# Kernel tuning notes

Hardware: AMD Instinct MI355X
Metric: run time of the kernel (lower is better)

The kernel has to match this reference:

```python
import jax, jax.numpy as jnp
import numpy as np

NUM_ROUTING = 3


def squash(s):
    # NOTE: original torch code sums the squared norm over axis=2 (the
    # out-capsule axis of s_j [B,1,O,Do]), NOT the feature axis. Faithful copy.
    norm = jnp.sum(s * s, axis=2, keepdims=True)
    scale = norm / (1.0 + norm) / jnp.sqrt(norm + 1e-9)
    return scale * s


def setup_inputs() -> dict:
    key = jax.random.key(0)
    k1, k2 = jax.random.split(key)
    B, N, Di, O, Do = 64, 8192, 8, 10, 16
    x = jax.random.normal(k1, (B, N, Di), dtype=jnp.float32)
    W = 0.01 * jax.random.normal(k2, (1, N, O, Do, Di), dtype=jnp.float32)
    return {"x": x, "W": W}


def reference(x, W):
    # x: [B, N, Di]; W: [1, N, O, Do, Di]
    N = x.shape[1]
    O = W.shape[2]
    # u_hat = W @ x per (n, o): [B, N, O, Do]
    u_hat = jnp.einsum('nodi,bni->bnod', W[0], x)
    b_ij = jnp.zeros((1, N, O, 1), dtype=x.dtype)
    v_j = None
    for r in range(NUM_ROUTING):
        c_ij = jax.nn.softmax(b_ij, axis=2)            # softmax over out caps
        s_j = jnp.sum(c_ij * u_hat, axis=1, keepdims=True)  # [B,1,O,Do]
        v_j = squash(s_j)
        if r < NUM_ROUTING - 1:
            # agreement: broadcasts b_ij to [B,N,O,1] after first update
            b_ij = b_ij + jnp.sum(u_hat * v_j, axis=-1, keepdims=True)
    return v_j[:, 0]  # [B, O, Do]
```

## Files before the change

### kernel.cpp

```cpp
#include <hip/hip_runtime.h>

typedef unsigned int u32;
typedef unsigned short u16;
typedef _Float16 h2 __attribute__((ext_vector_type(2)));
typedef _Float16 h4 __attribute__((ext_vector_type(4)));
typedef float f4 __attribute__((ext_vector_type(4)));

#define B_ 64
#define N_ 8192
#define DI 8
#define O_ 10
#define DO_ 16
#define OD 160
#define NB 256
#define NCH 32
#define WROW (OD * DI)
#define WLN (NCH * WROW)
#define XROW 264
#define CSTR 164

#define NCHUNK 8
#define CHN 2
#define NCHK (NCHUNK / CHN)
#define CHH (CHN * WROW)

static __device__ __forceinline__ h2 pkrtz(float a, float b) {
    return __builtin_bit_cast(h2, __builtin_amdgcn_cvt_pkrtz(a, b));
}

static __device__ __forceinline__ h2 hsum4(h2 v, int a32) {
    int pi = __builtin_bit_cast(int, v);
    h2 pk = v + __builtin_bit_cast(h2, __builtin_amdgcn_ds_swizzle(pi, 0x401F));
    pi = __builtin_bit_cast(int, pk);
    pk = pk + __builtin_bit_cast(h2, __builtin_amdgcn_ds_bpermute(a32, pi));
    return pk;
}

static __device__ __forceinline__ void gbar_arrive(u32* cnt, u32* flag, u32 k) {
    __syncthreads();
    if (threadIdx.x == 0) {
        const u32 old = __hip_atomic_fetch_add(cnt, 1u, __ATOMIC_RELEASE,
                                               __HIP_MEMORY_SCOPE_AGENT);
        if (old == k * NB - 1)
            __hip_atomic_store(flag, k, __ATOMIC_RELEASE, __HIP_MEMORY_SCOPE_AGENT);
    }
}
static __device__ __forceinline__ void gbar_wait(u32* flag, u32 k) {
    if (threadIdx.x == 0) {
        while (__hip_atomic_load(flag, __ATOMIC_RELAXED, __HIP_MEMORY_SCOPE_AGENT) < k)
            __builtin_amdgcn_s_sleep(8);
        (void)__hip_atomic_load(flag, __ATOMIC_ACQUIRE, __HIP_MEMORY_SCOPE_AGENT);
    }
    __syncthreads();
}

__global__ __launch_bounds__(512, 2)
void caps_fused(const float* __restrict__ Xf, const float* __restrict__ Wf,
                u32* bar, float* __restrict__ V0f, u16* __restrict__ Vb,
                _Float16* __restrict__ P, float* __restrict__ out) {
    __shared__ _Float16 wl[WLN];
    __shared__ _Float16 xl[B_ * XROW];
    __shared__ float cmb[B_ * CSTR];

    const int tid  = threadIdx.x;
    const int lane = tid & 63;
    const int c    = lane & 15;
    const int hh   = lane >> 4;
    const int w    = __builtin_amdgcn_readfirstlane(tid >> 6);
    const int tau  = w & 3, eta = w >> 2;
    const int b    = tau * 16 + c;
    const int bid  = blockIdx.x;
    const int nb   = bid * NCH;
    const int a32  = (lane ^ 32) << 2;
    const int ioff = (hh < 2) ? 4 * hh : 0;

    u32* cnt  = bar;
    u32* flag = bar + 32;

    {
        const float* src = Wf + (size_t)nb * WROW;
        float4 wv[20];
        #pragma unroll
        for (int k = 0; k < 20; ++k) wv[k] = *(const float4*)(src + (tid + k * 512) * 4);
        const float* xs = Xf + ((size_t)(tid >> 3) * N_ + nb) * DI;
        float4 xv[8];
        #pragma unroll
        for (int k = 0; k < 8; ++k) xv[k] = *(const float4*)(xs + ((tid & 7) + k * 8) * 4);
        #pragma unroll
        for (int k = 0; k < 20; ++k) {
            h2 lo = pkrtz(wv[k].x, wv[k].y), hi = pkrtz(wv[k].z, wv[k].w);
            h4 hv; hv[0] = lo[0]; hv[1] = lo[1]; hv[2] = hi[0]; hv[3] = hi[1];
            *(h4*)&wl[(tid + k * 512) * 4] = hv;
        }
        #pragma unroll
        for (int k = 0; k < 8; ++k) {
            const int pos = ((tid & 7) + k * 8) * 4;
            h2 lo = pkrtz(xv[k].x, xv[k].y), hi = pkrtz(xv[k].z, xv[k].w);
            h4 hv; hv[0] = lo[0]; hv[1] = lo[1]; hv[2] = hi[0]; hv[3] = hi[1];
            *(h4*)&xl[(tid >> 3) * XROW + pos] = hv;
        }
    }
    __syncthreads();

    const f4 fz = {0.f, 0.f, 0.f, 0.f};
    f4 acc[O_], vv[O_];
    const _Float16* xrow = xl + b * XROW + ioff;

    auto loadvv = [&]() {
        const _Float16* vp = (const _Float16*)Vb + (size_t)b * OD + 4 * hh;
        #pragma unroll
        for (int oo = 0; oo < O_; ++oo) {
            const h4 hv = *(const h4*)(vp + oo * DO_);
            vv[oo][0] = (float)hv[0]; vv[oo][1] = (float)hv[1];
            vv[oo][2] = (float)hv[2]; vv[oo][3] = (float)hv[3];
        }
    };

    auto step1 = [&](int sn) {
        h4 bf = {(_Float16)0.f, (_Float16)0.f, (_Float16)0.f, (_Float16)0.f};
        if (hh < 2) bf = *(const h4*)(xrow + sn * 8);
        const _Float16* wr = wl + sn * WROW + c * DI + ioff;
        f4 u[O_];
        #pragma unroll
        for (int oo = 0; oo < O_; ++oo) {
            h4 af = {(_Float16)0.f, (_Float16)0.f, (_Float16)0.f, (_Float16)0.f};
            if (hh < 2) af = *(const h4*)(wr + oo * (DO_ * DI));
            u[oo] = __builtin_amdgcn_mfma_f32_16x16x16f16(af, bf, fz, 0, 0, 0);
        }
        float tex[O_];
        #pragma unroll
        for (int q = 0; q < 5; ++q) {
            const int o0 = 2 * q, o1 = 2 * q + 1;
            const float p0 = u[o0][0]*vv[o0][0] + u[o0][1]*vv[o0][1]
                           + u[o0][2]*vv[o0][2] + u[o0][3]*vv[o0][3];
            const float p1 = u[o1][0]*vv[o1][0] + u[o1][1]*vv[o1][1]
                           + u[o1][2]*vv[o1][2] + u[o1][3]*vv[o1][3];
            const h2 pk = hsum4(pkrtz(p0, p1), a32);
            tex[o0] = __expf((float)pk[0]);
            tex[o1] = __expf((float)pk[1]);
        }
        const float den = (((tex[0] + tex[1]) + (tex[2] + tex[3]))
                         + ((tex[4] + tex[5]) + (tex[6] + tex[7])))
                         + (tex[8] + tex[9]);
        const float rinv = 1.0f / den;
        #pragma unroll
        for (int oo = 0; oo < O_; ++oo) {
            const float co = tex[oo] * rinv;
            acc[oo][0] = fmaf(co, u[oo][0], acc[oo][0]);
            acc[oo][1] = fmaf(co, u[oo][1], acc[oo][1]);
            acc[oo][2] = fmaf(co, u[oo][2], acc[oo][2]);
            acc[oo][3] = fmaf(co, u[oo][3], acc[oo][3]);
        }
    };

    auto epi = [&](float sc) {
        if (eta == 1) {
            #pragma unroll
            for (int oo = 0; oo < O_; ++oo)
                *(f4*)&cmb[b * CSTR + oo * DO_ + 4 * hh] = acc[oo];
        }
        __syncthreads();
        if (eta == 0) {
            _Float16* my = P + (size_t)bid * (B_ * OD) + (size_t)b * OD;
            #pragma unroll
            for (int oo = 0; oo < O_; ++oo) {
                const f4 t = acc[oo] + *(const f4*)&cmb[b * CSTR + oo * DO_ + 4 * hh];
                h4 hq;
                hq[0] = (_Float16)(sc * t[0]); hq[1] = (_Float16)(sc * t[1]);
                hq[2] = (_Float16)(sc * t[2]); hq[3] = (_Float16)(sc * t[3]);
                *(h4*)(my + oo * DO_ + 4 * hh) = hq;
            }
        }
    };

    auto reduceF = [&](int r) {
        float* sg = cmb;
        float* ss = cmb + 512;
        float* sca = cmb + 704;
        if (tid < 480) {
            const int g = tid / 160, od = tid - g * 160;
            float a2 = 0.0f;
            const _Float16* p0 = P + (size_t)bid * OD + od;
            #pragma unroll 8
            for (int p = g; p < NB; p += 3)
                a2 += (float)p0[(size_t)p * (B_ * OD)];
            sg[g * 160 + od] = a2;
        }
        __syncthreads();
        if (tid < 160) ss[tid] = sg[tid] + sg[160 + tid] + sg[320 + tid];
        __syncthreads();
        if (tid < 16) {
            float nrm = 0.0f;
            #pragma unroll
            for (int o = 0; o < O_; ++o) { const float x = ss[o * DO_ + tid]; nrm = fmaf(x, x, nrm); }
            sca[tid] = nrm / (1.0f + nrm) * rsqrtf(nrm + 1e-9f);
        }
        __syncthreads();
        if (tid < 160) {
            const float v = ss[tid] * sca[tid & 15];
            const int idx = bid * OD + tid;
            if (r == 0) {
                V0f[idx] = v;
                _Float16 hcv = (_Float16)v;
                Vb[idx] = __builtin_bit_cast(u16, hcv);
            } else if (r == 1) {
                _Float16 hcv = (_Float16)(V0f[idx] + v);
                Vb[idx] = __builtin_bit_cast(u16, hcv);
            } else {
                out[idx] = v;
            }
        }
        __syncthreads();
    };

    #pragma unroll
    for (int oo = 0; oo < O_; ++oo) acc[oo] = fz;
    #pragma unroll 1
    for (int st = 0; st < 16; ++st) {
        const int sn = eta * 16 + st;
        h4 bf = {(_Float16)0.f, (_Float16)0.f, (_Float16)0.f, (_Float16)0.f};
        if (hh < 2) bf = *(const h4*)(xrow + sn * 8);
        const _Float16* wr = wl + sn * WROW + c * DI + ioff;
        #pragma unroll
        for (int oo = 0; oo < O_; ++oo) {
            h4 af = {(_Float16)0.f, (_Float16)0.f, (_Float16)0.f, (_Float16)0.f};
            if (hh < 2) af = *(const h4*)(wr + oo * (DO_ * DI));
            acc[oo] = __builtin_amdgcn_mfma_f32_16x16x16f16(af, bf, acc[oo], 0, 0, 0);
        }
    }
    epi(0.1f);
    gbar_arrive(cnt, flag, 1); gbar_wait(flag, 1);
    if (bid < B_) reduceF(0);
    gbar_arrive(cnt, flag, 2); gbar_wait(flag, 2);
    loadvv();

    #pragma unroll
    for (int oo = 0; oo < O_; ++oo) acc[oo] = fz;
    #pragma unroll 1
    for (int st = 0; st < 16; ++st) step1(eta * 16 + st);
    epi(1.0f);
    gbar_arrive(cnt, flag, 3); gbar_wait(flag, 3);
    if (bid < B_) reduceF(1);
    gbar_arrive(cnt, flag, 4); gbar_wait(flag, 4);
    loadvv();

    #pragma unroll
    for (int oo = 0; oo < O_; ++oo) acc[oo] = fz;
    #pragma unroll 1
    for (int st = 0; st < 16; ++st) step1(eta * 16 + st);
    epi(1.0f);

    gbar_arrive(cnt, flag, 5);
    if (bid < B_) {
        gbar_wait(flag, 5);
        reduceF(2);
    }
}

template <int PHASE, int TAIL>
__global__ __launch_bounds__(256, 3)
void caps_pass(const float* __restrict__ Xf, const float* __restrict__ Wf,
               const u16* __restrict__ Vb, float* __restrict__ Sout,
               _Float16* __restrict__ Sh) {
    __shared__ _Float16 stage[2 * CHH];

    const int tid  = threadIdx.x;
    const int lane = tid & 63;
    const int c    = lane & 15;
    const int hh   = lane >> 4;
    const int tau  = __builtin_amdgcn_readfirstlane(tid >> 6);
    const int b    = tau * 16 + c;
    const int nb   = blockIdx.x * NCHUNK;
    const int a32  = (lane ^ 32) << 2;

    int off[5];
    #pragma unroll
    for (int k = 0; k < 5; ++k) off[k] = (tid + k * 256) * 2;

    float2 st[5];
    {
        const float* src = Wf + (size_t)nb * WROW;
        #pragma unroll
        for (int k = 0; k < 5; ++k) st[k] = *(const float2*)(src + off[k]);
        #pragma unroll
        for (int k = 0; k < 5; ++k)
            *(h2*)&stage[off[k]] = pkrtz(st[k].x, st[k].y);
    }

    f4 vv[O_];
    if (PHASE > 0) {
        const _Float16* vp = (const _Float16*)Vb + (size_t)b * OD + 4 * hh;
        #pragma unroll
        for (int oo = 0; oo < O_; ++oo) {
            const h4 hv = *(const h4*)(vp + oo * DO_);
            vv[oo][0] = (float)hv[0]; vv[oo][1] = (float)hv[1];
            vv[oo][2] = (float)hv[2]; vv[oo][3] = (float)hv[3];
        }
    }

    const f4 fz = {0.f, 0.f, 0.f, 0.f};
    f4 acc[O_];
    #pragma unroll
    for (int oo = 0; oo < O_; ++oo) acc[oo] = fz;

    const int ioff = (hh < 2) ? 4 * hh : 0;
    const float* xb = Xf + ((size_t)b * N_ + nb) * DI + ioff;
    float4 xcur = *(const float4*)xb;

    __syncthreads();

    #pragma unroll 1
    for (int ch = 0; ch < NCHK; ++ch) {
        if (ch < NCHK - 1) {
            const float* src = Wf + (size_t)(nb + (ch + 1) * CHN) * WROW;
            #pragma unroll
            for (int k = 0; k < 5; ++k) st[k] = *(const float2*)(src + off[k]);
        }
        const _Float16* wb = stage + (ch & 1) * CHH;

        #pragma unroll
        for (int kk = 0; kk < CHN; ++kk) {
            const int s = ch * CHN + kk;
            float4 xnext = xcur;
            if (s < NCHUNK - 1)
                xnext = *(const float4*)(xb + (size_t)(s + 1) * DI);

            h4 bf = {(_Float16)0.f, (_Float16)0.f, (_Float16)0.f, (_Float16)0.f};
            if (hh < 2) {
                const h2 lo = pkrtz(xcur.x, xcur.y);
                const h2 hi = pkrtz(xcur.z, xcur.w);
                bf[0] = lo[0]; bf[1] = lo[1]; bf[2] = hi[0]; bf[3] = hi[1];
            }
            xcur = xnext;

            const _Float16* wr = wb + kk * WROW + c * DI + ioff;
            f4 u[O_];
            #pragma unroll
            for (int oo = 0; oo < O_; ++oo) {
                h4 af = {(_Float16)0.f, (_Float16)0.f, (_Float16)0.f, (_Float16)0.f};
                if (hh < 2) af = *(const h4*)(wr + oo * (DO_ * DI));
                if (PHASE == 0) {
                    acc[oo] = __builtin_amdgcn_mfma_f32_16x16x16f16(af, bf, acc[oo], 0, 0, 0);
                } else {
                    u[oo] = __builtin_amdgcn_mfma_f32_16x16x16f16(af, bf, fz, 0, 0, 0);
                }
            }

            if (PHASE > 0) {
                float tex[O_];
                #pragma unroll
                for (int q = 0; q < 5; ++q) {
                    const int o0 = 2 * q, o1 = 2 * q + 1;
                    const float p0 = u[o0][0]*vv[o0][0] + u[o0][1]*vv[o0][1]
                                   + u[o0][2]*vv[o0][2] + u[o0][3]*vv[o0][3];
                    const float p1 = u[o1][0]*vv[o1][0] + u[o1][1]*vv[o1][1]
                                   + u[o1][2]*vv[o1][2] + u[o1][3]*vv[o1][3];
                    const h2 pk = hsum4(pkrtz(p0, p1), a32);
                    tex[o0] = __expf((float)pk[0]);
                    tex[o1] = __expf((float)pk[1]);
                }
                const float den = (((tex[0] + tex[1]) + (tex[2] + tex[3]))
                                 + ((tex[4] + tex[5]) + (tex[6] + tex[7])))
                                 + (tex[8] + tex[9]);
                const float rinv = 1.0f / den;
                #pragma unroll
                for (int oo = 0; oo < O_; ++oo) {
                    const float co = tex[oo] * rinv;
                    acc[oo][0] = fmaf(co, u[oo][0], acc[oo][0]);
                    acc[oo][1] = fmaf(co, u[oo][1], acc[oo][1]);
                    acc[oo][2] = fmaf(co, u[oo][2], acc[oo][2]);
                    acc[oo][3] = fmaf(co, u[oo][3], acc[oo][3]);
                }
            }
        }

        if (ch < NCHK - 1) {
            _Float16* dst = stage + ((ch + 1) & 1) * CHH;
            #pragma unroll
            for (int k = 0; k < 5; ++k)
                *(h2*)&dst[off[k]] = pkrtz(st[k].x, st[k].y);
        }
        __syncthreads();
    }

    const float sc = (PHASE == 0) ? 0.1f : 1.0f;
    {
        float* Sg = Sout + (size_t)b * OD;
        #pragma unroll
        for (int oo = 0; oo < O_; ++oo) {
            atomicAdd(&Sg[oo * DO_ + 4 * hh + 0], sc * acc[oo][0]);
            atomicAdd(&Sg[oo * DO_ + 4 * hh + 1], sc * acc[oo][1]);
            atomicAdd(&Sg[oo * DO_ + 4 * hh + 2], sc * acc[oo][2]);
            atomicAdd(&Sg[oo * DO_ + 4 * hh + 3], sc * acc[oo][3]);
        }
    }
    (void)Sh;
}

template <int PHASE>
__global__ __launch_bounds__(1024)
void caps_finalize(float* __restrict__ S, float* __restrict__ V0f,
                   u16* __restrict__ Vb, float* __restrict__ out) {
    const int tid = threadIdx.x;
    const int b = tid >> 4, d = tid & 15;
    float sv[O_];
    float norm = 0.0f;
    #pragma unroll
    for (int o = 0; o < O_; ++o) {
        sv[o] = S[b * OD + o * DO_ + d];
        norm = fmaf(sv[o], sv[o], norm);
    }
    const float scale = norm / (1.0f + norm) * rsqrtf(norm + 1e-9f);
    #pragma unroll
    for (int o = 0; o < O_; ++o) {
        const int idx = b * OD + o * DO_ + d;
        const float v = scale * sv[o];
        if (PHASE == 0) {
            V0f[idx] = v;
            _Float16 hcv = (_Float16)v;
            Vb[idx] = __builtin_bit_cast(u16, hcv);
            S[idx] = 0.0f;
        } else if (PHASE == 1) {
            _Float16 hcv = (_Float16)(V0f[idx] + v);
            Vb[idx] = __builtin_bit_cast(u16, hcv);
            S[idx] = 0.0f;
        } else {
            out[idx] = v;
        }
    }
}

extern "C" void kernel_launch(void* const* d_in, const int* in_sizes, int n_in,
                              void* d_out, int out_size, void* d_ws, size_t ws_size,
                              hipStream_t stream) {
    const float* Xf = (const float*)d_in[0];
    const float* Wf = (const float*)d_in[1];
    float* out = (float*)d_out;

    const size_t velems = (size_t)B_ * OD;
    float* V0f = (float*)d_ws;
    u16* Vb = (u16*)(V0f + velems);
    u32* bar = (u32*)((char*)d_ws + 61440);
    const size_t pbase = 61696;
    const size_t need = pbase + (size_t)NB * velems * 2;

    if (ws_size >= need) {
        _Float16* P = (_Float16*)((char*)d_ws + pbase);
        (void)hipMemsetAsync(bar, 0, 256, stream);
        caps_fused<<<dim3(NB), dim3(512), 0, stream>>>(Xf, Wf, bar, V0f, Vb, P, out);
    } else {
        float* S = (float*)((char*)d_ws + pbase);
        const dim3 grid(N_ / NCHUNK), blk(256), one(1), fblk(1024);
        (void)hipMemsetAsync(S, 0, velems * sizeof(float), stream);
        caps_pass<0, 2><<<grid, blk, 0, stream>>>(Xf, Wf, nullptr, S, nullptr);
        caps_finalize<0><<<one, fblk, 0, stream>>>(S, V0f, Vb, nullptr);
        caps_pass<1, 2><<<grid, blk, 0, stream>>>(Xf, Wf, Vb, S, nullptr);
        caps_finalize<1><<<one, fblk, 0, stream>>>(S, V0f, Vb, nullptr);
        caps_pass<1, 2><<<grid, blk, 0, stream>>>(Xf, Wf, Vb, S, nullptr);
        caps_finalize<2><<<one, fblk, 0, stream>>>(S, nullptr, nullptr, out);
    }
}
```

Measured before the change: 203.9 us.

## Double grid to 512 blocks with half chunk per block and tree barrier

```diff
diff --git a/kernel.cpp b/kernel.cpp
--- a/kernel.cpp
+++ b/kernel.cpp
@@ -12,12 +12,12 @@
 #define O_ 10
 #define DO_ 16
 #define OD 160
-#define NB 256
-#define NCH 32
+#define NB2 512
+#define NCH 16
 #define WROW (OD * DI)
 #define WLN (NCH * WROW)
-#define XROW 264
-#define CSTR 164
+#define XROWH 136
+#define CSTRH 164
 
 #define NCHUNK 8
 #define CHN 2
@@ -36,17 +36,25 @@
     return pk;
 }
 
-static __device__ __forceinline__ void gbar_arrive(u32* cnt, u32* flag, u32 k) {
+static __device__ __forceinline__ void gbar_arrive(u32* bar, u32 k) {
     __syncthreads();
     if (threadIdx.x == 0) {
-        const u32 old = __hip_atomic_fetch_add(cnt, 1u, __ATOMIC_RELEASE,
-                                               __HIP_MEMORY_SCOPE_AGENT);
-        if (old == k * NB - 1)
-            __hip_atomic_store(flag, k, __ATOMIC_RELEASE, __HIP_MEMORY_SCOPE_AGENT);
-    }
-}
-static __device__ __forceinline__ void gbar_wait(u32* flag, u32 k) {
+        u32* leaf = bar + (blockIdx.x & 7) * 32;
+        u32* root = bar + 8 * 32;
+        u32* flag = bar + 9 * 32;
+        const u32 lo = __hip_atomic_fetch_add(leaf, 1u, __ATOMIC_RELEASE,
+                                              __HIP_MEMORY_SCOPE_AGENT);
+        if (lo == k * (NB2 / 8) - 1) {
+            const u32 ro = __hip_atomic_fetch_add(root, 1u, __ATOMIC_RELEASE,
+                                                  __HIP_MEMORY_SCOPE_AGENT);
+            if (ro == k * 8 - 1)
+                __hip_atomic_store(flag, k, __ATOMIC_RELEASE, __HIP_MEMORY_SCOPE_AGENT);
+        }
+    }
+}
+static __device__ __forceinline__ void gbar_wait(u32* bar, u32 k) {
     if (threadIdx.x == 0) {
+        u32* flag = bar + 9 * 32;
         while (__hip_atomic_load(flag, __ATOMIC_RELAXED, __HIP_MEMORY_SCOPE_AGENT) < k)
             __builtin_amdgcn_s_sleep(8);
         (void)__hip_atomic_load(flag, __ATOMIC_ACQUIRE, __HIP_MEMORY_SCOPE_AGENT);
@@ -54,13 +62,13 @@
     __syncthreads();
 }
 
-__global__ __launch_bounds__(512, 2)
+__global__ __launch_bounds__(512, 4)
 void caps_fused(const float* __restrict__ Xf, const float* __restrict__ Wf,
                 u32* bar, float* __restrict__ V0f, u16* __restrict__ Vb,
                 _Float16* __restrict__ P, float* __restrict__ out) {
     __shared__ _Float16 wl[WLN];
-    __shared__ _Float16 xl[B_ * XROW];
-    __shared__ float cmb[B_ * CSTR];
+    __shared__ _Float16 xl[B_ * XROWH];
+    __shared__ alignas(16) _Float16 cmbh[B_ * CSTRH];
 
     const int tid  = threadIdx.x;
     const int lane = tid & 63;
@@ -74,37 +82,34 @@
     const int a32  = (lane ^ 32) << 2;
     const int ioff = (hh < 2) ? 4 * hh : 0;
 
-    u32* cnt  = bar;
-    u32* flag = bar + 32;
-
     {
         const float* src = Wf + (size_t)nb * WROW;
-        float4 wv[20];
-        #pragma unroll
-        for (int k = 0; k < 20; ++k) wv[k] = *(const float4*)(src + (tid + k * 512) * 4);
+        float4 wv[10];
+        #pragma unroll
+        for (int k = 0; k < 10; ++k) wv[k] = *(const float4*)(src + (tid + k * 512) * 4);
         const float* xs = Xf + ((size_t)(tid >> 3) * N_ + nb) * DI;
-        float4 xv[8];
-        #pragma unroll
-        for (int k = 0; k < 8; ++k) xv[k] = *(const float4*)(xs + ((tid & 7) + k * 8) * 4);
-        #pragma unroll
-        for (int k = 0; k < 20; ++k) {
+        float4 xv[4];
+        #pragma unroll
+        for (int k = 0; k < 4; ++k) xv[k] = *(const float4*)(xs + ((tid & 7) + k * 8) * 4);
+        #pragma unroll
+        for (int k = 0; k < 10; ++k) {
             h2 lo = pkrtz(wv[k].x, wv[k].y), hi = pkrtz(wv[k].z, wv[k].w);
             h4 hv; hv[0] = lo[0]; hv[1] = lo[1]; hv[2] = hi[0]; hv[3] = hi[1];
             *(h4*)&wl[(tid + k * 512) * 4] = hv;
         }
         #pragma unroll
-        for (int k = 0; k < 8; ++k) {
-            const int pos = ((tid & 7) + k * 8) * 4;
+        for (int k = 0; k < 4; ++k) {
+            const int idx = ((tid & 7) + k * 8) * 4;
             h2 lo = pkrtz(xv[k].x, xv[k].y), hi = pkrtz(xv[k].z, xv[k].w);
             h4 hv; hv[0] = lo[0]; hv[1] = lo[1]; hv[2] = hi[0]; hv[3] = hi[1];
-            *(h4*)&xl[(tid >> 3) * XROW + pos] = hv;
+            *(h4*)&xl[(tid >> 3) * XROWH + idx] = hv;
         }
     }
     __syncthreads();
 
     const f4 fz = {0.f, 0.f, 0.f, 0.f};
     f4 acc[O_], vv[O_];
-    const _Float16* xrow = xl + b * XROW + ioff;
+    const _Float16* xrow = xl + b * XROWH + ioff;
 
     auto loadvv = [&]() {
         const _Float16* vp = (const _Float16*)Vb + (size_t)b * OD + 4 * hh;
@@ -156,33 +161,40 @@
     auto epi = [&](float sc) {
         if (eta == 1) {
             #pragma unroll
-            for (int oo = 0; oo < O_; ++oo)
-                *(f4*)&cmb[b * CSTR + oo * DO_ + 4 * hh] = acc[oo];
+            for (int oo = 0; oo < O_; ++oo) {
+                h4 hp;
+                hp[0] = (_Float16)acc[oo][0]; hp[1] = (_Float16)acc[oo][1];
+                hp[2] = (_Float16)acc[oo][2]; hp[3] = (_Float16)acc[oo][3];
+                *(h4*)&cmbh[b * CSTRH + oo * DO_ + 4 * hh] = hp;
+            }
         }
         __syncthreads();
         if (eta == 0) {
             _Float16* my = P + (size_t)bid * (B_ * OD) + (size_t)b * OD;
             #pragma unroll
             for (int oo = 0; oo < O_; ++oo) {
-                const f4 t = acc[oo] + *(const f4*)&cmb[b * CSTR + oo * DO_ + 4 * hh];
+                const h4 hp = *(const h4*)&cmbh[b * CSTRH + oo * DO_ + 4 * hh];
                 h4 hq;
-                hq[0] = (_Float16)(sc * t[0]); hq[1] = (_Float16)(sc * t[1]);
-                hq[2] = (_Float16)(sc * t[2]); hq[3] = (_Float16)(sc * t[3]);
+                hq[0] = (_Float16)(sc * (acc[oo][0] + (float)hp[0]));
+                hq[1] = (_Float16)(sc * (acc[oo][1] + (float)hp[1]));
+                hq[2] = (_Float16)(sc * (acc[oo][2] + (float)hp[2]));
+                hq[3] = (_Float16)(sc * (acc[oo][3] + (float)hp[3]));
                 *(h4*)(my + oo * DO_ + 4 * hh) = hq;
             }
         }
+        __syncthreads();
     };
 
     auto reduceF = [&](int r) {
-        float* sg = cmb;
-        float* ss = cmb + 512;
-        float* sca = cmb + 704;
+        float* sg  = (float*)cmbh;
+        float* ss  = (float*)cmbh + 512;
+        float* sca = (float*)cmbh + 704;
         if (tid < 480) {
             const int g = tid / 160, od = tid - g * 160;
             float a2 = 0.0f;
             const _Float16* p0 = P + (size_t)bid * OD + od;
-            #pragma unroll 8
-            for (int p = g; p < NB; p += 3)
+            #pragma unroll 16
+            for (int p = g; p < NB2; p += 3)
                 a2 += (float)p0[(size_t)p * (B_ * OD)];
             sg[g * 160 + od] = a2;
         }
@@ -216,8 +228,8 @@
     #pragma unroll
     for (int oo = 0; oo < O_; ++oo) acc[oo] = fz;
     #pragma unroll 1
-    for (int st = 0; st < 16; ++st) {
-        const int sn = eta * 16 + st;
+    for (int st = 0; st < NCH / 2; ++st) {
+        const int sn = eta * (NCH / 2) + st;
         h4 bf = {(_Float16)0.f, (_Float16)0.f, (_Float16)0.f, (_Float16)0.f};
         if (hh < 2) bf = *(const h4*)(xrow + sn * 8);
         const _Float16* wr = wl + sn * WROW + c * DI + ioff;
@@ -229,30 +241,30 @@
         }
     }
     epi(0.1f);
-    gbar_arrive(cnt, flag, 1); gbar_wait(flag, 1);
+    gbar_arrive(bar, 1); gbar_wait(bar, 1);
     if (bid < B_) reduceF(0);
-    gbar_arrive(cnt, flag, 2); gbar_wait(flag, 2);
+    gbar_arrive(bar, 2); gbar_wait(bar, 2);
     loadvv();
 
     #pragma unroll
     for (int oo = 0; oo < O_; ++oo) acc[oo] = fz;
     #pragma unroll 1
-    for (int st = 0; st < 16; ++st) step1(eta * 16 + st);
+    for (int st = 0; st < NCH / 2; ++st) step1(eta * (NCH / 2) + st);
     epi(1.0f);
-    gbar_arrive(cnt, flag, 3); gbar_wait(flag, 3);
+    gbar_arrive(bar, 3); gbar_wait(bar, 3);
     if (bid < B_) reduceF(1);
-    gbar_arrive(cnt, flag, 4); gbar_wait(flag, 4);
+    gbar_arrive(bar, 4); gbar_wait(bar, 4);
     loadvv();
 
     #pragma unroll
     for (int oo = 0; oo < O_; ++oo) acc[oo] = fz;
     #pragma unroll 1
-    for (int st = 0; st < 16; ++st) step1(eta * 16 + st);
+    for (int st = 0; st < NCH / 2; ++st) step1(eta * (NCH / 2) + st);
     epi(1.0f);
 
-    gbar_arrive(cnt, flag, 5);
+    gbar_arrive(bar, 5);
     if (bid < B_) {
-        gbar_wait(flag, 5);
+        gbar_wait(bar, 5);
         reduceF(2);
     }
 }
@@ -441,13 +453,13 @@
     float* V0f = (float*)d_ws;
     u16* Vb = (u16*)(V0f + velems);
     u32* bar = (u32*)((char*)d_ws + 61440);
-    const size_t pbase = 61696;
-    const size_t need = pbase + (size_t)NB * velems * 2;
+    const size_t pbase = 62720;
+    const size_t need = pbase + (size_t)NB2 * velems * 2;
 
     if (ws_size >= need) {
         _Float16* P = (_Float16*)((char*)d_ws + pbase);
-        (void)hipMemsetAsync(bar, 0, 256, stream);
-        caps_fused<<<dim3(NB), dim3(512), 0, stream>>>(Xf, Wf, bar, V0f, Vb, P, out);
+        (void)hipMemsetAsync(bar, 0, 1280, stream);
+        caps_fused<<<dim3(NB2), dim3(512), 0, stream>>>(Xf, Wf, bar, V0f, Vb, P, out);
     } else {
         float* S = (float*)((char*)d_ws + pbase);
         const dim3 grid(N_ / NCHUNK), blk(256), one(1), fblk(1024);
```

Result: slower. 287.4 us (+41.0%).
